# Kernel tuning notes

Measured on AMD Instinct MI355X. Metric: run time of the kernel, lower is better.

## Reference

```python
import jax, jax.numpy as jnp
import numpy as np

K = 3        # kernel_size
PAD = 1      # padding
STRIDE = 1   # stride (must be 1: module asserts offset HxW == input HxW)
DIL = 1      # dilation


def _bilinear_gather(x, py, px):
    """x: (B,C,H,W); py,px: (B,KK,Ho,Wo) float sample coords.
    Returns (B,C,KK,Ho,Wo), zero outside bounds (DCNv2 semantics)."""
    B, C, H, W = x.shape
    y0 = jnp.floor(py); x0 = jnp.floor(px)
    wy1 = py - y0; wy0 = 1.0 - wy1
    wx1 = px - x0; wx0 = 1.0 - wx1
    flat = x.reshape(B, C, H * W)

    def gather(yi, xi):
        valid = (yi >= 0) & (yi < H) & (xi >= 0) & (xi < W)
        yc = jnp.clip(yi, 0, H - 1).astype(jnp.int32)
        xc = jnp.clip(xi, 0, W - 1).astype(jnp.int32)
        idx = (yc * W + xc).reshape(B, 1, -1)                      # (B,1,KK*Ho*Wo)
        g = jnp.take_along_axis(flat, jnp.broadcast_to(idx, (B, C, idx.shape[-1])), axis=2)
        g = g.reshape(B, C, *yi.shape[1:])                          # (B,C,KK,Ho,Wo)
        return jnp.where(valid[:, None], g, 0.0)

    v00 = gather(y0, x0)
    v01 = gather(y0, x0 + 1)
    v10 = gather(y0 + 1, x0)
    v11 = gather(y0 + 1, x0 + 1)
    wy0 = wy0[:, None]; wy1 = wy1[:, None]; wx0 = wx0[:, None]; wx1 = wx1[:, None]
    return wy0 * (wx0 * v00 + wx1 * v01) + wy1 * (wx0 * v10 + wx1 * v11)


def dcn_v2(x, coord_offset, coord_weight, weight, bias):
    B, C, H, W = x.shape
    O = weight.shape[0]
    KK = K * K
    # offset channels ordered (k, [y,x]) per DCNv2 layout
    offs = coord_offset.reshape(B, KK, 2, H, W)
    oy, ox = offs[:, :, 0], offs[:, :, 1]
    ky, kx = jnp.meshgrid(jnp.arange(K), jnp.arange(K), indexing='ij')
    ky = ky.reshape(KK); kx = kx.reshape(KK)
    # base sampling grid for each output pixel / kernel tap: (KK,H,W)
    py = (jnp.arange(H) * STRIDE - PAD)[None, :, None] + (ky * DIL)[:, None, None]
    px = (jnp.arange(W) * STRIDE - PAD)[None, None, :] + (kx * DIL)[:, None, None]
    py = py.astype(x.dtype)[None] + oy   # (B,KK,H,W)
    px = px.astype(x.dtype)[None] + ox
    sampled = _bilinear_gather(x, py, px)              # (B,C,KK,H,W)
    sampled = sampled * coord_weight[:, None]          # modulation mask
    out = jnp.einsum('bckhw,ock->bohw', sampled, weight.reshape(O, C, KK))
    return out + bias[None, :, None, None]


def setup_inputs() -> dict:
    key = jax.random.key(0)
    k1, k2, k3, k4, k5 = jax.random.split(key, 5)
    B, C, O, H, W = 8, 256, 256, 64, 64
    return {
        'input': jax.random.normal(k1, (B, C, H, W), dtype=jnp.float32),
        'coord_offset': jax.random.normal(k2, (B, 2 * K * K, H, W), dtype=jnp.float32),
        'coord_weight': jax.random.uniform(k3, (B, K * K, H, W), dtype=jnp.float32),
        'weight': jax.random.normal(k4, (O, C, K, K), dtype=jnp.float32) * 0.02,
        'bias': jax.random.normal(k5, (O,), dtype=jnp.float32) * 0.01,
    }


def reference(input, coord_offset, coord_weight, weight, bias):
    return dcn_v2(input, coord_offset, coord_weight, weight, bias)
```

## Files before the change

### kernel.cpp

```cpp
#include <hip/hip_runtime.h>
#include <hip/hip_bf16.h>
#include <stdint.h>

typedef __bf16 bf16_t;
typedef bf16_t bf16x8 __attribute__((ext_vector_type(8)));
typedef float f32x4 __attribute__((ext_vector_type(4)));
typedef float f32x2 __attribute__((ext_vector_type(2)));

__global__ __launch_bounds__(256) void k_transpose(const float* __restrict__ x,
                                                   bf16_t* __restrict__ xt) {
    __shared__ __align__(16) bf16_t tT[64][264];
    const int b = blockIdx.x >> 6;
    const int y = blockIdx.x & 63;
    const int t = threadIdx.x;

    const float* src = x + ((size_t)(b * 256) * 64 + y) * 64;
    const int x4 = (t & 15) * 4;
    const int cs = t >> 4;
#pragma unroll
    for (int cc = 0; cc < 256; cc += 16) {
        int c = cc + cs;
        float4 v = *(const float4*)(src + (size_t)c * 4096 + x4);
        tT[x4 + 0][c] = (bf16_t)v.x;
        tT[x4 + 1][c] = (bf16_t)v.y;
        tT[x4 + 2][c] = (bf16_t)v.z;
        tT[x4 + 3][c] = (bf16_t)v.w;
    }
    __syncthreads();
    bf16_t* dst = xt + ((size_t)(b * 64 + y) * 64) * 256;
#pragma unroll
    for (int i = 0; i < 8; ++i) {
        const int s = t + 256 * i;
        const int xx = s >> 5, cg = s & 31;
        *(bf16x8*)(dst + xx * 256 + cg * 8) = *(const bf16x8*)&tT[xx][cg * 8];
    }
}

__global__ __launch_bounds__(256) void k_pack_w(const float* __restrict__ w,
                                                bf16_t* __restrict__ Wp) {
    __shared__ float lw[8 * 2304];
    const int t = threadIdx.x;
    const int o0 = blockIdx.x * 8;
    const float4* src = (const float4*)(w + (size_t)o0 * 2304);
#pragma unroll
    for (int i = 0; i < 18; ++i) {
        ((float4*)lw)[t + 256 * i] = src[t + 256 * i];
    }
    __syncthreads();
#pragma unroll
    for (int i = 0; i < 9; ++i) {
        const int u = t + 256 * i;
        const int o = u / 288, r = u - o * 288;
        const int kb2 = r >> 3, rr = r & 7;
        const int s = rr >> 2, qq = rr & 3;
        const int kk = kb2 >> 2, cp = kb2 & 3;
        bf16x8 v;
#pragma unroll
        for (int e = 0; e < 8; ++e) {
            const int c = cp * 64 + s * 32 + qq * 8 + e;
            v[e] = (bf16_t)lw[o * 2304 + c * 9 + kk];
        }
        *(bf16x8*)(Wp + ((size_t)(kb2 * 2 + s) * 256 + o0 + o) * 32 + qq * 8) = v;
    }
}

__global__ __launch_bounds__(512, 4) void k_dcn(
    const bf16_t* __restrict__ xt, const bf16_t* __restrict__ Wp,
    const float* __restrict__ coff, const float* __restrict__ cwm,
    const float* __restrict__ bias, float* __restrict__ out) {

    __shared__ __align__(16) bf16_t sS[2][64 * 64];
    __shared__ float sCW[9][4][64];
    __shared__ int   sCA[9][4][64];

    const int blk = blockIdx.x;
    const int b  = blk & 7;
    const int h  = blk >> 3;
    const int t = threadIdx.x;
    const int wv = t >> 6;
    const int lane = t & 63;

    const int p = t >> 3;
    const int q = t & 7;

    const int fr = lane & 15;
    const int quad = lane >> 4;
    const int swz = fr & 7;

    for (int u = t; u < 576; u += 512) {
        const int kk = u >> 6, wpx = u & 63;
        float oy = coff[((size_t)(b * 18 + kk * 2 + 0) * 64 + h) * 64 + wpx];
        float ox = coff[((size_t)(b * 18 + kk * 2 + 1) * 64 + h) * 64 + wpx];
        float m  = cwm [((size_t)(b * 9 + kk) * 64 + h) * 64 + wpx];
        float py = (float)(h - 1 + (kk / 3)) + oy;
        float px = (float)(wpx - 1 + (kk % 3)) + ox;
        float fy = floorf(py), fx = floorf(px);
        int y0 = (int)fy, x0 = (int)fx;
        int y1 = y0 + 1,  x1 = x0 + 1;
        float wy1 = py - fy, wx1 = px - fx;
        float wy0 = 1.0f - wy1, wx0 = 1.0f - wx1;
        bool vy0 = (y0 >= 0) && (y0 < 64), vy1 = (y1 >= 0) && (y1 < 64);
        bool vx0 = (x0 >= 0) && (x0 < 64), vx1 = (x1 >= 0) && (x1 < 64);
        int yc0 = min(max(y0, 0), 63), yc1 = min(max(y1, 0), 63);
        int xc0 = min(max(x0, 0), 63), xc1 = min(max(x1, 0), 63);
        const int base = b * 4096;
        sCW[kk][0][wpx] = (vy0 && vx0) ? wy0 * wx0 * m : 0.0f;
        sCW[kk][1][wpx] = (vy0 && vx1) ? wy0 * wx1 * m : 0.0f;
        sCW[kk][2][wpx] = (vy1 && vx0) ? wy1 * wx0 * m : 0.0f;
        sCW[kk][3][wpx] = (vy1 && vx1) ? wy1 * wx1 * m : 0.0f;
        sCA[kk][0][wpx] = (base + yc0 * 64 + xc0) * 256;
        sCA[kk][1][wpx] = (base + yc0 * 64 + xc1) * 256;
        sCA[kk][2][wpx] = (base + yc1 * 64 + xc0) * 256;
        sCA[kk][3][wpx] = (base + yc1 * 64 + xc1) * 256;
    }
    __syncthreads();

    const bf16_t* wA = Wp + (wv * 32 + fr) * 32 + quad * 8;
    bf16_t* sSw0 = &sS[0][0] + p * 64 + ((q ^ (p & 7)) * 8);

    f32x4 acc[2][4] = {};
    bf16x8 aC[2][2], aN[2][2];

    auto sample_into = [&](int iter, int buf) {
        const int kk = iter >> 2, cp = iter & 3;
        const float w0 = sCW[kk][0][p], w1 = sCW[kk][1][p];
        const float w2 = sCW[kk][2][p], w3 = sCW[kk][3][p];
        const int cb = cp * 64 + q * 8;
        bf16x8 g0 = *(const bf16x8*)(xt + sCA[kk][0][p] + cb);
        bf16x8 g1 = *(const bf16x8*)(xt + sCA[kk][1][p] + cb);
        bf16x8 g2 = *(const bf16x8*)(xt + sCA[kk][2][p] + cb);
        bf16x8 g3 = *(const bf16x8*)(xt + sCA[kk][3][p] + cb);
        f32x2 s2[4] = {};
        f32x2 W0 = {w0, w0}, W1 = {w1, w1}, W2 = {w2, w2}, W3 = {w3, w3};
#pragma unroll
        for (int j = 0; j < 4; ++j) {
            f32x2 f0 = {(float)g0[2 * j], (float)g0[2 * j + 1]};
            f32x2 f1 = {(float)g1[2 * j], (float)g1[2 * j + 1]};
            f32x2 f2 = {(float)g2[2 * j], (float)g2[2 * j + 1]};
            f32x2 f3 = {(float)g3[2 * j], (float)g3[2 * j + 1]};
            s2[j] += W0 * f0; s2[j] += W1 * f1; s2[j] += W2 * f2; s2[j] += W3 * f3;
        }
        bf16x8 ov;
#pragma unroll
        for (int j = 0; j < 4; ++j) {
            ov[2 * j]     = (bf16_t)s2[j][0];
            ov[2 * j + 1] = (bf16_t)s2[j][1];
        }
        *(bf16x8*)(sSw0 + buf * 4096) = ov;
    };

    auto do_mfma = [&](int cur) {
        const bf16_t* sb = &sS[cur][0];
#pragma unroll
        for (int s = 0; s < 2; ++s) {
            const int coffe = ((s * 4 + quad) ^ swz) * 8;
            bf16x8 bb[4];
#pragma unroll
            for (int nt = 0; nt < 4; ++nt)
                bb[nt] = *(const bf16x8*)(sb + (nt * 16 + fr) * 64 + coffe);
#pragma unroll
            for (int mt = 0; mt < 2; ++mt)
#pragma unroll
                for (int nt = 0; nt < 4; ++nt)
                    acc[mt][nt] = __builtin_amdgcn_mfma_f32_16x16x32_bf16(
                        aC[mt][s], bb[nt], acc[mt][nt], 0, 0, 0);
        }
    };

    sample_into(0, 0);
    aC[0][0] = *(const bf16x8*)(wA);
    aC[0][1] = *(const bf16x8*)(wA + 8192);
    aC[1][0] = *(const bf16x8*)(wA + 512);
    aC[1][1] = *(const bf16x8*)(wA + 8192 + 512);
    __syncthreads();

    for (int iter = 0; iter < 36; ++iter) {
        const int cur = iter & 1;
        if (iter < 35) {
            const bf16_t* wn = wA + (size_t)(iter + 1) * 16384;
            aN[0][0] = *(const bf16x8*)(wn);
            aN[0][1] = *(const bf16x8*)(wn + 8192);
            aN[1][0] = *(const bf16x8*)(wn + 512);
            aN[1][1] = *(const bf16x8*)(wn + 8192 + 512);
            sample_into(iter + 1, 1 - cur);
            do_mfma(cur);
#pragma unroll
            for (int mt = 0; mt < 2; ++mt)
#pragma unroll
                for (int s = 0; s < 2; ++s) aC[mt][s] = aN[mt][s];
        } else {
            do_mfma(cur);
        }
        __syncthreads();
    }

    const int rowq = quad * 4;
#pragma unroll
    for (int mt = 0; mt < 2; ++mt) {
#pragma unroll
        for (int r = 0; r < 4; ++r) {
            const int og = wv * 32 + mt * 16 + rowq + r;
            const float bs = bias[og];
            float* op = out + ((size_t)(b * 256 + og) * 64 + h) * 64;
#pragma unroll
            for (int nt = 0; nt < 4; ++nt) {
                op[nt * 16 + fr] = acc[mt][nt][r] + bs;
            }
        }
    }
}

extern "C" void kernel_launch(void* const* d_in, const int* in_sizes, int n_in,
                              void* d_out, int out_size, void* d_ws, size_t ws_size,
                              hipStream_t stream) {
    const float* x    = (const float*)d_in[0];
    const float* coff = (const float*)d_in[1];
    const float* cwm  = (const float*)d_in[2];
    const float* wgt  = (const float*)d_in[3];
    const float* bias = (const float*)d_in[4];
    float* out = (float*)d_out;

    bf16_t* xt = (bf16_t*)d_ws;
    bf16_t* Wp = xt + (size_t)8 * 64 * 64 * 256;

    k_transpose<<<512, 256, 0, stream>>>(x, xt);
    k_pack_w   <<<32,  256, 0, stream>>>(wgt, Wp);
    k_dcn      <<<512, 512, 0, stream>>>(xt, Wp, coff, cwm, bias, out);
}
```

Baseline: 153.9 us.

## Switch to fp16 with packed-half bilinear blend, fused prep kernel, interleaved gather/MFMA

```diff
diff --git a/kernel.cpp b/kernel.cpp
--- a/kernel.cpp
+++ b/kernel.cpp
@@ -2,76 +2,80 @@
 #include <hip/hip_bf16.h>
 #include <stdint.h>
 
-typedef __bf16 bf16_t;
-typedef bf16_t bf16x8 __attribute__((ext_vector_type(8)));
+typedef _Float16 f16_t;
+typedef f16_t f16x8 __attribute__((ext_vector_type(8)));
+typedef f16_t f16x2 __attribute__((ext_vector_type(2)));
 typedef float f32x4 __attribute__((ext_vector_type(4)));
-typedef float f32x2 __attribute__((ext_vector_type(2)));
-
-__global__ __launch_bounds__(256) void k_transpose(const float* __restrict__ x,
-                                                   bf16_t* __restrict__ xt) {
-    __shared__ __align__(16) bf16_t tT[64][264];
-    const int b = blockIdx.x >> 6;
-    const int y = blockIdx.x & 63;
+
+__device__ inline f16x2 as_f16x2(int v) {
+    union { int i; f16x2 h; } u; u.i = v; return u.h;
+}
+
+__global__ __launch_bounds__(256) void k_prep(const float* __restrict__ x,
+                                              const float* __restrict__ w,
+                                              f16_t* __restrict__ xt,
+                                              f16_t* __restrict__ Wp) {
+    __shared__ __align__(16) char smem[36864];
     const int t = threadIdx.x;
-
-    const float* src = x + ((size_t)(b * 256) * 64 + y) * 64;
-    const int x4 = (t & 15) * 4;
-    const int cs = t >> 4;
-#pragma unroll
-    for (int cc = 0; cc < 256; cc += 16) {
-        int c = cc + cs;
-        float4 v = *(const float4*)(src + (size_t)c * 4096 + x4);
-        tT[x4 + 0][c] = (bf16_t)v.x;
-        tT[x4 + 1][c] = (bf16_t)v.y;
-        tT[x4 + 2][c] = (bf16_t)v.z;
-        tT[x4 + 3][c] = (bf16_t)v.w;
-    }
-    __syncthreads();
-    bf16_t* dst = xt + ((size_t)(b * 64 + y) * 64) * 256;
-#pragma unroll
-    for (int i = 0; i < 8; ++i) {
-        const int s = t + 256 * i;
-        const int xx = s >> 5, cg = s & 31;
-        *(bf16x8*)(dst + xx * 256 + cg * 8) = *(const bf16x8*)&tT[xx][cg * 8];
-    }
-}
-
-__global__ __launch_bounds__(256) void k_pack_w(const float* __restrict__ w,
-                                                bf16_t* __restrict__ Wp) {
-    __shared__ float lw[8 * 2304];
-    const int t = threadIdx.x;
-    const int o0 = blockIdx.x * 8;
-    const float4* src = (const float4*)(w + (size_t)o0 * 2304);
-#pragma unroll
-    for (int i = 0; i < 18; ++i) {
-        ((float4*)lw)[t + 256 * i] = src[t + 256 * i];
-    }
-    __syncthreads();
-#pragma unroll
-    for (int i = 0; i < 9; ++i) {
-        const int u = t + 256 * i;
-        const int o = u / 288, r = u - o * 288;
-        const int kb2 = r >> 3, rr = r & 7;
-        const int s = rr >> 2, qq = rr & 3;
-        const int kk = kb2 >> 2, cp = kb2 & 3;
-        bf16x8 v;
-#pragma unroll
-        for (int e = 0; e < 8; ++e) {
-            const int c = cp * 64 + s * 32 + qq * 8 + e;
-            v[e] = (bf16_t)lw[o * 2304 + c * 9 + kk];
-        }
-        *(bf16x8*)(Wp + ((size_t)(kb2 * 2 + s) * 256 + o0 + o) * 32 + qq * 8) = v;
+    if (blockIdx.x < 512) {
+        f16_t (*tT)[264] = (f16_t(*)[264])smem;
+        const int b = blockIdx.x >> 6;
+        const int y = blockIdx.x & 63;
+        const float* src = x + ((size_t)(b * 256) * 64 + y) * 64;
+        const int x4 = (t & 15) * 4;
+        const int cs = t >> 4;
+#pragma unroll
+        for (int cc = 0; cc < 256; cc += 16) {
+            int c = cc + cs;
+            float4 v = *(const float4*)(src + (size_t)c * 4096 + x4);
+            tT[x4 + 0][c] = (f16_t)v.x;
+            tT[x4 + 1][c] = (f16_t)v.y;
+            tT[x4 + 2][c] = (f16_t)v.z;
+            tT[x4 + 3][c] = (f16_t)v.w;
+        }
+        __syncthreads();
+        f16_t* dst = xt + ((size_t)(b * 64 + y) * 64) * 256;
+#pragma unroll
+        for (int i = 0; i < 8; ++i) {
+            const int s = t + 256 * i;
+            const int xx = s >> 5, cg = s & 31;
+            *(f16x8*)(dst + xx * 256 + cg * 8) = *(const f16x8*)&tT[xx][cg * 8];
+        }
+    } else {
+        float* lw = (float*)smem;
+        const int o0 = (blockIdx.x - 512) * 4;
+        const float4* src = (const float4*)(w + (size_t)o0 * 2304);
+#pragma unroll
+        for (int i = 0; i < 9; ++i)
+            ((float4*)lw)[t + 256 * i] = src[t + 256 * i];
+        __syncthreads();
+#pragma unroll
+        for (int i = 0; i < 5; ++i) {
+            const int u = t + 256 * i;
+            if (u < 1152) {
+                const int o = u / 288, r = u - o * 288;
+                const int kb2 = r >> 3, rr = r & 7;
+                const int s = rr >> 2, qq = rr & 3;
+                const int kk = kb2 >> 2, cp = kb2 & 3;
+                f16x8 v;
+#pragma unroll
+                for (int e = 0; e < 8; ++e) {
+                    const int c = cp * 64 + s * 32 + qq * 8 + e;
+                    v[e] = (f16_t)lw[o * 2304 + c * 9 + kk];
+                }
+                *(f16x8*)(Wp + ((size_t)(kb2 * 2 + s) * 256 + o0 + o) * 32 + qq * 8) = v;
+            }
+        }
     }
 }
 
 __global__ __launch_bounds__(512, 4) void k_dcn(
-    const bf16_t* __restrict__ xt, const bf16_t* __restrict__ Wp,
+    const f16_t* __restrict__ xt, const f16_t* __restrict__ Wp,
     const float* __restrict__ coff, const float* __restrict__ cwm,
     const float* __restrict__ bias, float* __restrict__ out) {
 
-    __shared__ __align__(16) bf16_t sS[2][64 * 64];
-    __shared__ float sCW[9][4][64];
-    __shared__ int   sCA[9][4][64];
+    __shared__ __align__(16) f16_t sS[2][64 * 64];
+    __shared__ __align__(16) int2 sT[9 * 64 * 4];
 
     const int blk = blockIdx.x;
     const int b  = blk & 7;
@@ -104,86 +108,110 @@
         int yc0 = min(max(y0, 0), 63), yc1 = min(max(y1, 0), 63);
         int xc0 = min(max(x0, 0), 63), xc1 = min(max(x1, 0), 63);
         const int base = b * 4096;
-        sCW[kk][0][wpx] = (vy0 && vx0) ? wy0 * wx0 * m : 0.0f;
-        sCW[kk][1][wpx] = (vy0 && vx1) ? wy0 * wx1 * m : 0.0f;
-        sCW[kk][2][wpx] = (vy1 && vx0) ? wy1 * wx0 * m : 0.0f;
-        sCW[kk][3][wpx] = (vy1 && vx1) ? wy1 * wx1 * m : 0.0f;
-        sCA[kk][0][wpx] = (base + yc0 * 64 + xc0) * 256;
-        sCA[kk][1][wpx] = (base + yc0 * 64 + xc1) * 256;
-        sCA[kk][2][wpx] = (base + yc1 * 64 + xc0) * 256;
-        sCA[kk][3][wpx] = (base + yc1 * 64 + xc1) * 256;
+        float cw[4];
+        int   ca[4];
+        cw[0] = (vy0 && vx0) ? wy0 * wx0 * m : 0.0f;
+        cw[1] = (vy0 && vx1) ? wy0 * wx1 * m : 0.0f;
+        cw[2] = (vy1 && vx0) ? wy1 * wx0 * m : 0.0f;
+        cw[3] = (vy1 && vx1) ? wy1 * wx1 * m : 0.0f;
+        ca[0] = (base + yc0 * 64 + xc0) * 512;
+        ca[1] = (base + yc0 * 64 + xc1) * 512;
+        ca[2] = (base + yc1 * 64 + xc0) * 512;
+        ca[3] = (base + yc1 * 64 + xc1) * 512;
+#pragma unroll
+        for (int c = 0; c < 4; ++c) {
+            union { unsigned short us; f16_t hh; } cv;
+            cv.hh = (f16_t)cw[c];
+            int wp = (int)cv.us | ((int)cv.us << 16);
+            sT[(kk * 64 + wpx) * 4 + c] = make_int2(ca[c], wp);
+        }
     }
     __syncthreads();
 
-    const bf16_t* wA = Wp + (wv * 32 + fr) * 32 + quad * 8;
-    bf16_t* sSw0 = &sS[0][0] + p * 64 + ((q ^ (p & 7)) * 8);
+    const f16_t* wA = Wp + (wv * 32 + fr) * 32 + quad * 8;
+    f16_t* sw0 = &sS[0][p * 64 + ((q ^ (p & 7)) * 8)];
+    f16_t* sw1 = sw0 + 4096;
+    const int qb = q * 16;
 
     f32x4 acc[2][4] = {};
-    bf16x8 aC[2][2], aN[2][2];
-
-    auto sample_into = [&](int iter, int buf) {
-        const int kk = iter >> 2, cp = iter & 3;
-        const float w0 = sCW[kk][0][p], w1 = sCW[kk][1][p];
-        const float w2 = sCW[kk][2][p], w3 = sCW[kk][3][p];
-        const int cb = cp * 64 + q * 8;
-        bf16x8 g0 = *(const bf16x8*)(xt + sCA[kk][0][p] + cb);
-        bf16x8 g1 = *(const bf16x8*)(xt + sCA[kk][1][p] + cb);
-        bf16x8 g2 = *(const bf16x8*)(xt + sCA[kk][2][p] + cb);
-        bf16x8 g3 = *(const bf16x8*)(xt + sCA[kk][3][p] + cb);
-        f32x2 s2[4] = {};
-        f32x2 W0 = {w0, w0}, W1 = {w1, w1}, W2 = {w2, w2}, W3 = {w3, w3};
-#pragma unroll
-        for (int j = 0; j < 4; ++j) {
-            f32x2 f0 = {(float)g0[2 * j], (float)g0[2 * j + 1]};
-            f32x2 f1 = {(float)g1[2 * j], (float)g1[2 * j + 1]};
-            f32x2 f2 = {(float)g2[2 * j], (float)g2[2 * j + 1]};
-            f32x2 f3 = {(float)g3[2 * j], (float)g3[2 * j + 1]};
-            s2[j] += W0 * f0; s2[j] += W1 * f1; s2[j] += W2 * f2; s2[j] += W3 * f3;
-        }
-        bf16x8 ov;
-#pragma unroll
-        for (int j = 0; j < 4; ++j) {
-            ov[2 * j]     = (bf16_t)s2[j][0];
-            ov[2 * j + 1] = (bf16_t)s2[j][1];
-        }
-        *(bf16x8*)(sSw0 + buf * 4096) = ov;
+    f16x8 aC[2][2], aN[2][2];
+
+    auto loadA = [&](int it, f16x8 (&a)[2][2]) {
+        const f16_t* wn = wA + (size_t)it * 16384;
+        a[0][0] = *(const f16x8*)(wn);
+        a[0][1] = *(const f16x8*)(wn + 8192);
+        a[1][0] = *(const f16x8*)(wn + 512);
+        a[1][1] = *(const f16x8*)(wn + 8192 + 512);
     };
 
     auto do_mfma = [&](int cur) {
-        const bf16_t* sb = &sS[cur][0];
+        const f16_t* sb = &sS[cur][0];
 #pragma unroll
         for (int s = 0; s < 2; ++s) {
             const int coffe = ((s * 4 + quad) ^ swz) * 8;
-            bf16x8 bb[4];
+            f16x8 bb[4];
 #pragma unroll
             for (int nt = 0; nt < 4; ++nt)
-                bb[nt] = *(const bf16x8*)(sb + (nt * 16 + fr) * 64 + coffe);
+                bb[nt] = *(const f16x8*)(sb + (nt * 16 + fr) * 64 + coffe);
 #pragma unroll
             for (int mt = 0; mt < 2; ++mt)
 #pragma unroll
                 for (int nt = 0; nt < 4; ++nt)
-                    acc[mt][nt] = __builtin_amdgcn_mfma_f32_16x16x32_bf16(
+                    acc[mt][nt] = __builtin_amdgcn_mfma_f32_16x16x32_f16(
                         aC[mt][s], bb[nt], acc[mt][nt], 0, 0, 0);
         }
     };
 
-    sample_into(0, 0);
-    aC[0][0] = *(const bf16x8*)(wA);
-    aC[0][1] = *(const bf16x8*)(wA + 8192);
-    aC[1][0] = *(const bf16x8*)(wA + 512);
-    aC[1][1] = *(const bf16x8*)(wA + 8192 + 512);
+    {
+        const int2* e = &sT[p * 4];
+        int2 e0 = e[0], e1 = e[1], e2 = e[2], e3 = e[3];
+        const char* xb = (const char*)xt;
+        f16x8 g0 = *(const f16x8*)(xb + (e0.x + qb));
+        f16x8 g1 = *(const f16x8*)(xb + (e1.x + qb));
+        f16x8 g2 = *(const f16x8*)(xb + (e2.x + qb));
+        f16x8 g3 = *(const f16x8*)(xb + (e3.x + qb));
+        f16x2 w0 = as_f16x2(e0.y), w1 = as_f16x2(e1.y);
+        f16x2 w2 = as_f16x2(e2.y), w3 = as_f16x2(e3.y);
+        const f16x2* g0p = (const f16x2*)&g0;
+        const f16x2* g1p = (const f16x2*)&g1;
+        const f16x2* g2p = (const f16x2*)&g2;
+        const f16x2* g3p = (const f16x2*)&g3;
+        f16x8 ov; f16x2* op = (f16x2*)&ov;
+#pragma unroll
+        for (int j = 0; j < 4; ++j)
+            op[j] = g0p[j] * w0 + g1p[j] * w1 + g2p[j] * w2 + g3p[j] * w3;
+        *(f16x8*)sw0 = ov;
+    }
+    loadA(0, aC);
     __syncthreads();
 
-    for (int iter = 0; iter < 36; ++iter) {
-        const int cur = iter & 1;
-        if (iter < 35) {
-            const bf16_t* wn = wA + (size_t)(iter + 1) * 16384;
-            aN[0][0] = *(const bf16x8*)(wn);
-            aN[0][1] = *(const bf16x8*)(wn + 8192);
-            aN[1][0] = *(const bf16x8*)(wn + 512);
-            aN[1][1] = *(const bf16x8*)(wn + 8192 + 512);
-            sample_into(iter + 1, 1 - cur);
+#pragma unroll 2
+    for (int it = 0; it < 36; ++it) {
+        const int cur = it & 1;
+        if (it < 35) {
+            const int nx = it + 1;
+            const int kk = nx >> 2, cp = nx & 3;
+            const int2* e = &sT[(kk * 64 + p) * 4];
+            int2 e0 = e[0], e1 = e[1], e2 = e[2], e3 = e[3];
+            const int cb = cp * 128 + qb;
+            const char* xb = (const char*)xt;
+            f16x8 g0 = *(const f16x8*)(xb + (e0.x + cb));
+            f16x8 g1 = *(const f16x8*)(xb + (e1.x + cb));
+            f16x8 g2 = *(const f16x8*)(xb + (e2.x + cb));
+            f16x8 g3 = *(const f16x8*)(xb + (e3.x + cb));
+            loadA(nx, aN);
             do_mfma(cur);
+            f16x2 w0 = as_f16x2(e0.y), w1 = as_f16x2(e1.y);
+            f16x2 w2 = as_f16x2(e2.y), w3 = as_f16x2(e3.y);
+            const f16x2* g0p = (const f16x2*)&g0;
+            const f16x2* g1p = (const f16x2*)&g1;
+            const f16x2* g2p = (const f16x2*)&g2;
+            const f16x2* g3p = (const f16x2*)&g3;
+            f16x8 ov; f16x2* op = (f16x2*)&ov;
+#pragma unroll
+            for (int j = 0; j < 4; ++j)
+                op[j] = g0p[j] * w0 + g1p[j] * w1 + g2p[j] * w2 + g3p[j] * w3;
+            *(f16x8*)(cur ? sw0 : sw1) = ov;
 #pragma unroll
             for (int mt = 0; mt < 2; ++mt)
 #pragma unroll
@@ -201,10 +229,10 @@
         for (int r = 0; r < 4; ++r) {
             const int og = wv * 32 + mt * 16 + rowq + r;
             const float bs = bias[og];
-            float* op = out + ((size_t)(b * 256 + og) * 64 + h) * 64;
+            float* opn = out + ((size_t)(b * 256 + og) * 64 + h) * 64;
 #pragma unroll
             for (int nt = 0; nt < 4; ++nt) {
-                op[nt * 16 + fr] = acc[mt][nt][r] + bs;
+                opn[nt * 16 + fr] = acc[mt][nt][r] + bs;
             }
         }
     }
@@ -220,10 +248,9 @@
     const float* bias = (const float*)d_in[4];
     float* out = (float*)d_out;
 
-    bf16_t* xt = (bf16_t*)d_ws;
-    bf16_t* Wp = xt + (size_t)8 * 64 * 64 * 256;
-
-    k_transpose<<<512, 256, 0, stream>>>(x, xt);
-    k_pack_w   <<<32,  256, 0, stream>>>(wgt, Wp);
-    k_dcn      <<<512, 512, 0, stream>>>(xt, Wp, coff, cwm, bias, out);
-}
+    f16_t* xt = (f16_t*)d_ws;
+    f16_t* Wp = xt + (size_t)8 * 64 * 64 * 256;
+
+    k_prep<<<576, 256, 0, stream>>>(x, wgt, xt, Wp);
+    k_dcn <<<512, 512, 0, stream>>>(xt, Wp, coff, cwm, bias, out);
+}
```

After: 153.3 us. Within noise of the previous version (-0.4%).
